# Kernel optimization log

Measured on AMD Instinct MI355X. Metric: run time of the kernel, lower is better.

Reference implementation:

```python
import jax, jax.numpy as jnp
import numpy as np


def setup_inputs() -> dict:
    key = jax.random.key(0)
    ks = jax.random.split(key, 6)
    B, T, S, E, D = 8, 128, 512, 512, 512  # batch, trg_len, src_len, enc_dim, trg_dim
    W_SCALE = 0.03  # small init to keep tanh unsaturated
    return {
        "hidden": jax.random.normal(ks[0], (B, T, D), jnp.float32),
        "encoder_outputs": jax.random.normal(ks[1], (B, S, E), jnp.float32),
        "encoder_mask": jnp.ones((B, S), jnp.float32),
        "W_attn": jax.random.normal(ks[2], (D, E + D), jnp.float32) * W_SCALE,
        "b_attn": jnp.zeros((D,), jnp.float32),
        "W_v": jax.random.normal(ks[3], (1, D), jnp.float32) * W_SCALE,
        "b_v": jnp.zeros((1,), jnp.float32),
        "W_out": jax.random.normal(ks[4], (D, E + D), jnp.float32) * W_SCALE,
    }


def masked_softmax(x, m, axis=-1):
    # faithful to repo: x*m, stable exp, e*m, normalize with eps
    x = x * m
    e_x = jnp.exp(x - jnp.max(x, axis=axis, keepdims=True))
    e_x = e_x * m
    return e_x / (jnp.sum(e_x, axis=axis, keepdims=True) + 1e-6)


def reference(hidden, encoder_outputs, encoder_mask, W_attn, b_attn, W_v, b_v, W_out):
    B, T, D = hidden.shape
    S = encoder_outputs.shape[1]
    # concat order in get_energy is (hidden_i, encoder_outputs), so split W_attn
    W_h = W_attn[:, :D]   # (D_out, trg_dim)
    W_e = W_attn[:, D:]   # (D_out, enc_dim)
    # Linear(concat) == h@W_h^T + e@W_e^T + b; vectorized over all (t, s) pairs
    hp = jnp.einsum('btd,kd->btk', hidden, W_h)            # (B,T,K)
    ep = jnp.einsum('bse,ke->bsk', encoder_outputs, W_e)   # (B,S,K)
    feat = jnp.tanh(hp[:, :, None, :] + ep[:, None, :, :] + b_attn)  # (B,T,S,K)
    energies = jnp.einsum('btsk,k->bts', feat, W_v[0]) + b_v[0]      # (B,T,S)
    # forward: energies * mask, then masked softmax
    m = encoder_mask[:, None, :]  # (B,1,S)
    energies = energies * m
    attn_weights = masked_softmax(energies, m, axis=-1)    # (B,T,S)
    weighted_context = jnp.einsum('bts,bse->bte', attn_weights, encoder_outputs)
    h_cat = jnp.concatenate([weighted_context, hidden], axis=-1)  # (B,T,E+D)
    h_tilde = jnp.tanh(jnp.einsum('btc,dc->btd', h_cat, W_out))   # (B,T,D)
    return h_tilde, weighted_context, attn_weights
```

## Files before the change

### kernel.cpp

```cpp
#include <hip/hip_runtime.h>
#include <hip/hip_bf16.h>
#include <math.h>

typedef unsigned short u16;
typedef unsigned int u32;
typedef __bf16 bf16x8 __attribute__((ext_vector_type(8)));
typedef float f32x4 __attribute__((ext_vector_type(4)));

#define OUT_WC   524288LL
#define OUT_ATTN 1048576LL
#define C2 2.8853900817779268f
#define LOG2E 1.4426950408889634f
#define LAS 40

__device__ inline u16 f2b(float f) {
    return (u16)((__float_as_uint(f) + 0x8000u) >> 16);
}
__device__ inline u32 pkcvt(float x, float y) {
    __hip_bfloat162 h = __float22bfloat162_rn(make_float2(x, y));
    return *(u32*)&h;
}
__device__ inline float tanh_fast(float x) {
    return 1.f - 2.f * __builtin_amdgcn_rcpf(__builtin_amdgcn_exp2f(C2 * x) + 1.f);
}

__global__ __launch_bounds__(256) void tobf(
    const float* __restrict__ enc, const float* __restrict__ hidden,
    const float* __restrict__ Wattn, const float* __restrict__ Wout,
    u16* __restrict__ dst)
{
    long long i = ((long long)blockIdx.x * 256 + threadIdx.x) * 8;
    const float* src; long long off;
    if (i < 2097152)      { src = enc;    off = i; }
    else if (i < 2621440) { src = hidden; off = i - 2097152; }
    else if (i < 3145728) { src = Wattn;  off = i - 2621440; }
    else                  { src = Wout;   off = i - 3145728; }
    float4 v0 = *(const float4*)(src + off);
    float4 v1 = *(const float4*)(src + off + 4);
    *(uint4*)(dst + i) = make_uint4(pkcvt(v0.x, v0.y), pkcvt(v0.z, v0.w),
                                    pkcvt(v1.x, v1.y), pkcvt(v1.z, v1.w));
}

__global__ __launch_bounds__(256) void proj(
    const u16* __restrict__ hidden_bf, const u16* __restrict__ enc_bf,
    const u16* __restrict__ Wattn_bf, const float* __restrict__ battn,
    const u16* __restrict__ Wout_bf,
    float* __restrict__ hp, u16* __restrict__ ept, float* __restrict__ hh)
{
    __shared__ u16 lA[64 * LAS];
    __shared__ u16 lB[64 * LAS];
    const int tid = threadIdx.x;
    const int wvi = tid >> 6, ln = tid & 63;
    const int wm = wvi >> 1, wn = wvi & 1;
    const int l16 = ln & 15, quad = ln >> 4;
    const int blk = blockIdx.x;
    int bx, by, zz = 0, lda, ldb, mode;
    const u16 *A, *B;
    if (blk < 512) {
        mode = 0;
        zz = blk >> 6; by = (blk >> 3) & 7; bx = blk & 7;
        A = Wattn_bf + 512; lda = 1024;
        B = enc_bf + (long long)zz * 262144; ldb = 512;
    } else if (blk < 640) {
        mode = 1;
        int i = blk - 512; by = i >> 3; bx = i & 7;
        A = hidden_bf; lda = 512;
        B = Wattn_bf; ldb = 1024;
    } else {
        mode = 2;
        int i = blk - 640; by = i >> 3; bx = i & 7;
        A = hidden_bf; lda = 512;
        B = Wout_bf + 512; ldb = 1024;
    }
    const int m0 = by * 64, n0 = bx * 64;
    const int srow = tid >> 2, skof = (tid & 3) * 8;
    const u16* Ap = A + (long long)(m0 + srow) * lda + skof;
    const u16* Bp = B + (long long)(n0 + srow) * ldb + skof;

    f32x4 acc00 = {0,0,0,0}, acc01 = {0,0,0,0}, acc10 = {0,0,0,0}, acc11 = {0,0,0,0};

    for (int k0 = 0; k0 < 512; k0 += 32) {
        uint4 av = *(const uint4*)(Ap + k0);
        uint4 bv = *(const uint4*)(Bp + k0);
        __syncthreads();
        *(uint4*)&lA[srow * LAS + skof] = av;
        *(uint4*)&lB[srow * LAS + skof] = bv;
        __syncthreads();
        bf16x8 a0 = *(const bf16x8*)&lA[(wm * 32      + l16) * LAS + quad * 8];
        bf16x8 a1 = *(const bf16x8*)&lA[(wm * 32 + 16 + l16) * LAS + quad * 8];
        bf16x8 b0 = *(const bf16x8*)&lB[(wn * 32      + l16) * LAS + quad * 8];
        bf16x8 b1 = *(const bf16x8*)&lB[(wn * 32 + 16 + l16) * LAS + quad * 8];
        acc00 = __builtin_amdgcn_mfma_f32_16x16x32_bf16(a0, b0, acc00, 0, 0, 0);
        acc01 = __builtin_amdgcn_mfma_f32_16x16x32_bf16(a0, b1, acc01, 0, 0, 0);
        acc10 = __builtin_amdgcn_mfma_f32_16x16x32_bf16(a1, b0, acc10, 0, 0, 0);
        acc11 = __builtin_amdgcn_mfma_f32_16x16x32_bf16(a1, b1, acc11, 0, 0, 0);
    }

    const f32x4* accs[4] = { &acc00, &acc01, &acc10, &acc11 };
    #pragma unroll
    for (int i = 0; i < 2; ++i) {
        #pragma unroll
        for (int j = 0; j < 2; ++j) {
            const f32x4& a = *accs[i * 2 + j];
            #pragma unroll
            for (int r = 0; r < 4; ++r) {
                int m = m0 + wm * 32 + i * 16 + quad * 4 + r;
                int n = n0 + wn * 32 + j * 16 + l16;
                float v = a[r];
                if (mode == 0)
                    ept[(long long)zz * 262144 + (long long)m * 512 + n] =
                        f2b(__builtin_amdgcn_exp2f(C2 * v));
                else if (mode == 1)
                    hp[(long long)m * 512 + n] = C2 * (v + battn[n]);
                else
                    hh[(long long)m * 512 + n] = v;
            }
        }
    }
}

__device__ inline float wred_sum(float v) {
    #pragma unroll
    for (int i = 32; i > 0; i >>= 1) v += __shfl_xor(v, i);
    return v;
}
__device__ inline float wred_max(float v) {
    #pragma unroll
    for (int i = 32; i > 0; i >>= 1) v = fmaxf(v, __shfl_xor(v, i));
    return v;
}

__device__ inline void proc8p(uint4 c0, uint4 c1, float4 hw0, float4 hw1,
                              float* a0, float* a1) {
    u32 p[4] = {c0.x, c0.y, c0.z, c0.w};
    u32 q[4] = {c1.x, c1.y, c1.z, c1.w};
    #pragma unroll
    for (int i = 0; i < 4; ++i) {
        float x0l = __uint_as_float(p[i] << 16);
        float x0h = __uint_as_float(p[i] & 0xFFFF0000u);
        float x1l = __uint_as_float(q[i] << 16);
        float x1h = __uint_as_float(q[i] & 0xFFFF0000u);
        float A, B, num;
        A = fmaf(hw0.x, x0l, 1.f);
        B = fmaf(hw1.x, x1l, 1.f);
        num = fmaf(hw0.z, B, hw1.z * A);
        a0[2*i]   = fmaf(num, __builtin_amdgcn_rcpf(A * B), a0[2*i]);
        A = fmaf(hw0.x, x0h, 1.f);
        B = fmaf(hw1.x, x1h, 1.f);
        num = fmaf(hw0.z, B, hw1.z * A);
        a0[2*i+1] = fmaf(num, __builtin_amdgcn_rcpf(A * B), a0[2*i+1]);
        A = fmaf(hw0.y, x0l, 1.f);
        B = fmaf(hw1.y, x1l, 1.f);
        num = fmaf(hw0.z, B, hw1.z * A);
        a1[2*i]   = fmaf(num, __builtin_amdgcn_rcpf(A * B), a1[2*i]);
        A = fmaf(hw0.y, x0h, 1.f);
        B = fmaf(hw1.y, x1h, 1.f);
        num = fmaf(hw0.z, B, hw1.z * A);
        a1[2*i+1] = fmaf(num, __builtin_amdgcn_rcpf(A * B), a1[2*i+1]);
    }
}
__device__ inline void wcproc2(uint4 c, float2 ap, float* acc0, float* acc1) {
    u32 cc[4] = {c.x, c.y, c.z, c.w};
    #pragma unroll
    for (int i = 0; i < 4; ++i) {
        float el = __uint_as_float(cc[i] << 16);
        float eh = __uint_as_float(cc[i] & 0xFFFF0000u);
        acc0[2*i]   = fmaf(ap.x, el, acc0[2*i]);
        acc0[2*i+1] = fmaf(ap.x, eh, acc0[2*i+1]);
        acc1[2*i]   = fmaf(ap.y, el, acc1[2*i]);
        acc1[2*i+1] = fmaf(ap.y, eh, acc1[2*i+1]);
    }
}

__global__ __launch_bounds__(1024) void energies(
    const float* __restrict__ maskp, const float* __restrict__ hp,
    const u16* __restrict__ ept, const float* __restrict__ Wv,
    const float* __restrict__ bvp, const u16* __restrict__ enc_bf,
    float* __restrict__ attn, float* __restrict__ wc)
{
    __shared__ __align__(16) float4 hpw[512];
    __shared__ float pa[2][16][512];
    __shared__ float aL[512][2];
    __shared__ float red[16];
    const int tid = threadIdx.x;
    const int b  = blockIdx.x & 7;
    const int t0 = (blockIdx.x >> 3) * 2;
    const int th = tid >> 9;
    const int k5 = tid & 511;
    const long long row0 = (long long)(b * 128 + t0) * 512;

    float hv = hp[row0 + (long long)th * 512 + k5];
    float eh = __builtin_amdgcn_exp2f(hv);
    float* hpwf = (float*)hpw;
    hpwf[k5 * 4 + th] = eh;
    float w = 0.f;
    if (th == 0) { w = Wv[k5]; hpwf[k5 * 4 + 2] = w; }
    float wsum = wred_sum(w);
    if ((tid & 63) == 0) red[tid >> 6] = wsum;
    __syncthreads();
    float sumWv = 0.f;
    #pragma unroll
    for (int i = 0; i < 16; ++i) sumWv += red[i];

    const int kg = tid >> 6, sl = tid & 63;
    const int s0 = sl * 8;
    const u16* eb = ept + (long long)b * 262144 + (kg * 32) * 512 + s0;
    const float4* hq = &hpw[kg * 32];

    float a0[8] = {0,0,0,0,0,0,0,0}, a1[8] = {0,0,0,0,0,0,0,0};
    uint4 c0 = *(const uint4*)(eb);
    uint4 c1 = *(const uint4*)(eb + 512);
    for (int kk = 0; kk < 30; kk += 2) {
        const u16* nb = eb + (kk + 2) * 512;
        uint4 n0 = *(const uint4*)(nb);
        uint4 n1 = *(const uint4*)(nb + 512);
        proc8p(c0, c1, hq[kk], hq[kk + 1], a0, a1);
        c0 = n0; c1 = n1;
    }
    proc8p(c0, c1, hq[30], hq[31], a0, a1);

    *(float4*)&pa[0][kg][s0]     = make_float4(a0[0], a0[1], a0[2], a0[3]);
    *(float4*)&pa[0][kg][s0 + 4] = make_float4(a0[4], a0[5], a0[6], a0[7]);
    *(float4*)&pa[1][kg][s0]     = make_float4(a1[0], a1[1], a1[2], a1[3]);
    *(float4*)&pa[1][kg][s0 + 4] = make_float4(a1[4], a1[5], a1[6], a1[7]);
    __syncthreads();

    float A = 0.f;
    #pragma unroll
    for (int g = 0; g < 16; ++g) A += pa[th][g][k5];
    float mv = maskp[(long long)b * 512 + k5];
    float bv0 = bvp[0];
    float r = (bv0 + sumWv - 2.f * A) * mv; r *= mv;

    float vmax = wred_max(r);
    if ((tid & 63) == 0) red[tid >> 6] = vmax;
    __syncthreads();
    float mx = red[th * 8];
    #pragma unroll
    for (int i = 1; i < 8; ++i) mx = fmaxf(mx, red[th * 8 + i]);

    float ex = __builtin_amdgcn_exp2f((r - mx) * LOG2E) * mv;
    float vsum = wred_sum(ex);
    __syncthreads();
    if ((tid & 63) == 0) red[tid >> 6] = vsum;
    __syncthreads();
    float sm = 0.f;
    #pragma unroll
    for (int i = 0; i < 8; ++i) sm += red[th * 8 + i];
    float at = ex * (1.f / (sm + 1e-6f));
    attn[row0 + (long long)th * 512 + k5] = at;
    aL[k5][th] = at;
    __syncthreads();

    const int eg = tid & 63, sg = tid >> 6;
    const u16* encb = enc_bf + (long long)b * 262144 + (long long)(sg * 32) * 512 + eg * 8;
    const float2* aq = (const float2*)&aL[sg * 32][0];
    float acc0[8] = {0,0,0,0,0,0,0,0}, acc1[8] = {0,0,0,0,0,0,0,0};
    uint4 e0 = *(const uint4*)(encb);
    uint4 e1 = *(const uint4*)(encb + 512);
    for (int j = 0; j < 30; j += 2) {
        uint4 f0 = *(const uint4*)(encb + (long long)(j + 2) * 512);
        uint4 f1 = *(const uint4*)(encb + (long long)(j + 3) * 512);
        wcproc2(e0, aq[j],     acc0, acc1);
        wcproc2(e1, aq[j + 1], acc0, acc1);
        e0 = f0; e1 = f1;
    }
    wcproc2(e0, aq[30], acc0, acc1);
    wcproc2(e1, aq[31], acc0, acc1);

    *(float4*)&pa[0][sg][eg * 8]     = make_float4(acc0[0], acc0[1], acc0[2], acc0[3]);
    *(float4*)&pa[0][sg][eg * 8 + 4] = make_float4(acc0[4], acc0[5], acc0[6], acc0[7]);
    *(float4*)&pa[1][sg][eg * 8]     = make_float4(acc1[0], acc1[1], acc1[2], acc1[3]);
    *(float4*)&pa[1][sg][eg * 8 + 4] = make_float4(acc1[4], acc1[5], acc1[6], acc1[7]);
    __syncthreads();

    float wcv = 0.f;
    #pragma unroll
    for (int g = 0; g < 16; ++g) wcv += pa[th][g][k5];
    wc[row0 + (long long)th * 512 + k5] = wcv;
}

__global__ __launch_bounds__(256) void hout_k(
    const float* __restrict__ wc, const u16* __restrict__ Wout_bf,
    float* __restrict__ out)
{
    __shared__ u16 lA[32 * LAS];
    __shared__ u16 lB[64 * LAS];
    const int tid = threadIdx.x;
    const int wvi = tid >> 6, ln = tid & 63;
    const int l16 = ln & 15, quad = ln >> 4;
    const int msub = wvi & 1, npair = wvi >> 1;
    const int m0 = blockIdx.y * 32, n0 = blockIdx.x * 64;
    const int rowA = tid >> 3, kofA = (tid & 7) * 4;
    const int rowB = tid >> 2, kofB = (tid & 3) * 8;
    f32x4 acc0 = {0,0,0,0}, acc1 = {0,0,0,0};

    for (int k0 = 0; k0 < 512; k0 += 32) {
        float4 av = *(const float4*)(wc + (long long)(m0 + rowA) * 512 + k0 + kofA);
        uint4 bv = *(const uint4*)(Wout_bf + (long long)(n0 + rowB) * 1024 + k0 + kofB);
        __syncthreads();
        *(uint2*)&lA[rowA * LAS + kofA] = make_uint2(pkcvt(av.x, av.y), pkcvt(av.z, av.w));
        int kk = kofB ^ (((rowB >> 3) & 3) << 3);
        *(uint4*)&lB[rowB * LAS + kk] = bv;
        __syncthreads();
        bf16x8 a = *(const bf16x8*)&lA[(msub * 16 + l16) * LAS + quad * 8];
        int nr0 = npair * 32 + l16, nr1 = nr0 + 16;
        bf16x8 b0 = *(const bf16x8*)&lB[nr0 * LAS + (quad * 8 ^ (((nr0 >> 3) & 3) << 3))];
        bf16x8 b1 = *(const bf16x8*)&lB[nr1 * LAS + (quad * 8 ^ (((nr1 >> 3) & 3) << 3))];
        acc0 = __builtin_amdgcn_mfma_f32_16x16x32_bf16(a, b0, acc0, 0, 0, 0);
        acc1 = __builtin_amdgcn_mfma_f32_16x16x32_bf16(a, b1, acc1, 0, 0, 0);
    }
    #pragma unroll
    for (int j = 0; j < 2; ++j) {
        const f32x4& a = j ? acc1 : acc0;
        #pragma unroll
        for (int r = 0; r < 4; ++r) {
            int m = m0 + msub * 16 + quad * 4 + r;
            int n = n0 + npair * 32 + j * 16 + l16;
            long long idx = (long long)m * 512 + n;
            out[idx] = tanh_fast(a[r] + out[idx]);
        }
    }
}

extern "C" void kernel_launch(void* const* d_in, const int* in_sizes, int n_in,
                              void* d_out, int out_size, void* d_ws, size_t ws_size,
                              hipStream_t stream)
{
    const float* hidden = (const float*)d_in[0];
    const float* enc    = (const float*)d_in[1];
    const float* mask   = (const float*)d_in[2];
    const float* Wattn  = (const float*)d_in[3];
    const float* battn  = (const float*)d_in[4];
    const float* Wv     = (const float*)d_in[5];
    const float* bvp    = (const float*)d_in[6];
    const float* Wout   = (const float*)d_in[7];
    float* out = (float*)d_out;

    float* hp  = (float*)d_ws;
    u16*   ept = (u16*)((char*)d_ws + (2 << 20));
    u16*   bfp = (u16*)((char*)d_ws + (6 << 20));
    u16* enc_bf    = bfp;
    u16* hidden_bf = bfp + 2097152;
    u16* Wattn_bf  = bfp + 2621440;
    u16* Wout_bf   = bfp + 3145728;

    tobf<<<1792, 256, 0, stream>>>(enc, hidden, Wattn, Wout, bfp);
    proj<<<768, 256, 0, stream>>>(hidden_bf, enc_bf, Wattn_bf, battn, Wout_bf,
                                  hp, ept, out );
    energies<<<512, 1024, 0, stream>>>(mask, hp, ept, Wv, bvp, enc_bf,
                                       out + OUT_ATTN, out + OUT_WC);
    hout_k<<<dim3(8, 32, 1), 256, 0, stream>>>(out + OUT_WC, Wout_bf, out);
}
```

Measured before the change: 140.1 us.

## Halve energies block size and shrink shared reduction buffer

The energies kernel now runs with 512 threads per block instead of 1024. Each thread handles 64 k-rows (or s-rows) instead of 32 and owns both target rows in the softmax stage. The shared partial-sum buffer shrinks from 2x16x512 to 8x512 floats by reducing the two rows in sequence with extra barriers, and the max and sum reductions are done for both rows together. The aim is lower LDS use and shorter cross-wave reductions so more blocks fit per CU, at the cost of longer serial loops and more syncs per block.

```diff
diff --git a/kernel.cpp b/kernel.cpp
--- a/kernel.cpp
+++ b/kernel.cpp
@@ -124,10 +124,32 @@
     for (int i = 32; i > 0; i >>= 1) v += __shfl_xor(v, i);
     return v;
 }
-__device__ inline float wred_max(float v) {
-    #pragma unroll
-    for (int i = 32; i > 0; i >>= 1) v = fmaxf(v, __shfl_xor(v, i));
-    return v;
+__device__ inline void bred2_max(float v0, float v1, float* red, int tid,
+                                 float* o0, float* o1) {
+    #pragma unroll
+    for (int i = 32; i > 0; i >>= 1) {
+        v0 = fmaxf(v0, __shfl_xor(v0, i));
+        v1 = fmaxf(v1, __shfl_xor(v1, i));
+    }
+    __syncthreads();
+    if ((tid & 63) == 0) { red[tid >> 6] = v0; red[8 + (tid >> 6)] = v1; }
+    __syncthreads();
+    float a0 = red[0], a1 = red[8];
+    #pragma unroll
+    for (int i = 1; i < 8; ++i) { a0 = fmaxf(a0, red[i]); a1 = fmaxf(a1, red[8 + i]); }
+    *o0 = a0; *o1 = a1;
+}
+__device__ inline void bred2_sum(float v0, float v1, float* red, int tid,
+                                 float* o0, float* o1) {
+    #pragma unroll
+    for (int i = 32; i > 0; i >>= 1) { v0 += __shfl_xor(v0, i); v1 += __shfl_xor(v1, i); }
+    __syncthreads();
+    if ((tid & 63) == 0) { red[tid >> 6] = v0; red[8 + (tid >> 6)] = v1; }
+    __syncthreads();
+    float a0 = 0.f, a1 = 0.f;
+    #pragma unroll
+    for (int i = 0; i < 8; ++i) { a0 += red[i]; a1 += red[8 + i]; }
+    *o0 = a0; *o1 = a1;
 }
 
 __device__ inline void proc8p(uint4 c0, uint4 c1, float4 hw0, float4 hw1,
@@ -172,112 +194,112 @@
     }
 }
 
-__global__ __launch_bounds__(1024) void energies(
+__global__ __launch_bounds__(512) void energies(
     const float* __restrict__ maskp, const float* __restrict__ hp,
     const u16* __restrict__ ept, const float* __restrict__ Wv,
     const float* __restrict__ bvp, const u16* __restrict__ enc_bf,
     float* __restrict__ attn, float* __restrict__ wc)
 {
     __shared__ __align__(16) float4 hpw[512];
-    __shared__ float pa[2][16][512];
+    __shared__ float pa[8][512];
     __shared__ float aL[512][2];
     __shared__ float red[16];
     const int tid = threadIdx.x;
     const int b  = blockIdx.x & 7;
     const int t0 = (blockIdx.x >> 3) * 2;
-    const int th = tid >> 9;
-    const int k5 = tid & 511;
     const long long row0 = (long long)(b * 128 + t0) * 512;
 
-    float hv = hp[row0 + (long long)th * 512 + k5];
-    float eh = __builtin_amdgcn_exp2f(hv);
-    float* hpwf = (float*)hpw;
-    hpwf[k5 * 4 + th] = eh;
-    float w = 0.f;
-    if (th == 0) { w = Wv[k5]; hpwf[k5 * 4 + 2] = w; }
+    float hv0 = hp[row0 + tid];
+    float hv1 = hp[row0 + 512 + tid];
+    float w = Wv[tid];
+    hpw[tid] = make_float4(__builtin_amdgcn_exp2f(hv0),
+                           __builtin_amdgcn_exp2f(hv1), w, 0.f);
     float wsum = wred_sum(w);
     if ((tid & 63) == 0) red[tid >> 6] = wsum;
     __syncthreads();
     float sumWv = 0.f;
     #pragma unroll
-    for (int i = 0; i < 16; ++i) sumWv += red[i];
+    for (int i = 0; i < 8; ++i) sumWv += red[i];
 
     const int kg = tid >> 6, sl = tid & 63;
     const int s0 = sl * 8;
-    const u16* eb = ept + (long long)b * 262144 + (kg * 32) * 512 + s0;
-    const float4* hq = &hpw[kg * 32];
+    const u16* eb = ept + (long long)b * 262144 + (kg * 64) * 512 + s0;
+    const float4* hq = &hpw[kg * 64];
 
     float a0[8] = {0,0,0,0,0,0,0,0}, a1[8] = {0,0,0,0,0,0,0,0};
     uint4 c0 = *(const uint4*)(eb);
     uint4 c1 = *(const uint4*)(eb + 512);
-    for (int kk = 0; kk < 30; kk += 2) {
+    for (int kk = 0; kk < 62; kk += 2) {
         const u16* nb = eb + (kk + 2) * 512;
         uint4 n0 = *(const uint4*)(nb);
         uint4 n1 = *(const uint4*)(nb + 512);
         proc8p(c0, c1, hq[kk], hq[kk + 1], a0, a1);
         c0 = n0; c1 = n1;
     }
-    proc8p(c0, c1, hq[30], hq[31], a0, a1);
-
-    *(float4*)&pa[0][kg][s0]     = make_float4(a0[0], a0[1], a0[2], a0[3]);
-    *(float4*)&pa[0][kg][s0 + 4] = make_float4(a0[4], a0[5], a0[6], a0[7]);
-    *(float4*)&pa[1][kg][s0]     = make_float4(a1[0], a1[1], a1[2], a1[3]);
-    *(float4*)&pa[1][kg][s0 + 4] = make_float4(a1[4], a1[5], a1[6], a1[7]);
-    __syncthreads();
-
-    float A = 0.f;
-    #pragma unroll
-    for (int g = 0; g < 16; ++g) A += pa[th][g][k5];
-    float mv = maskp[(long long)b * 512 + k5];
+    proc8p(c0, c1, hq[62], hq[63], a0, a1);
+
+    *(float4*)&pa[kg][s0]     = make_float4(a0[0], a0[1], a0[2], a0[3]);
+    *(float4*)&pa[kg][s0 + 4] = make_float4(a0[4], a0[5], a0[6], a0[7]);
+    __syncthreads();
+    float A0 = 0.f, A1 = 0.f;
+    #pragma unroll
+    for (int g = 0; g < 8; ++g) A0 += pa[g][tid];
+    __syncthreads();
+    *(float4*)&pa[kg][s0]     = make_float4(a1[0], a1[1], a1[2], a1[3]);
+    *(float4*)&pa[kg][s0 + 4] = make_float4(a1[4], a1[5], a1[6], a1[7]);
+    __syncthreads();
+    #pragma unroll
+    for (int g = 0; g < 8; ++g) A1 += pa[g][tid];
+
+    const int s = tid;
+    float mv = maskp[(long long)b * 512 + s];
     float bv0 = bvp[0];
-    float r = (bv0 + sumWv - 2.f * A) * mv; r *= mv;
-
-    float vmax = wred_max(r);
-    if ((tid & 63) == 0) red[tid >> 6] = vmax;
-    __syncthreads();
-    float mx = red[th * 8];
-    #pragma unroll
-    for (int i = 1; i < 8; ++i) mx = fmaxf(mx, red[th * 8 + i]);
-
-    float ex = __builtin_amdgcn_exp2f((r - mx) * LOG2E) * mv;
-    float vsum = wred_sum(ex);
-    __syncthreads();
-    if ((tid & 63) == 0) red[tid >> 6] = vsum;
-    __syncthreads();
-    float sm = 0.f;
-    #pragma unroll
-    for (int i = 0; i < 8; ++i) sm += red[th * 8 + i];
-    float at = ex * (1.f / (sm + 1e-6f));
-    attn[row0 + (long long)th * 512 + k5] = at;
-    aL[k5][th] = at;
+    float r0 = (bv0 + sumWv - 2.f * A0) * mv; r0 *= mv;
+    float r1 = (bv0 + sumWv - 2.f * A1) * mv; r1 *= mv;
+
+    float mx0, mx1;
+    bred2_max(r0, r1, red, tid, &mx0, &mx1);
+    float ex0 = __builtin_amdgcn_exp2f((r0 - mx0) * LOG2E) * mv;
+    float ex1 = __builtin_amdgcn_exp2f((r1 - mx1) * LOG2E) * mv;
+    float sm0, sm1;
+    bred2_sum(ex0, ex1, red, tid, &sm0, &sm1);
+    float at0 = ex0 * (1.f / (sm0 + 1e-6f));
+    float at1 = ex1 * (1.f / (sm1 + 1e-6f));
+    attn[row0 + s]       = at0;
+    attn[row0 + 512 + s] = at1;
+    aL[s][0] = at0; aL[s][1] = at1;
     __syncthreads();
 
     const int eg = tid & 63, sg = tid >> 6;
-    const u16* encb = enc_bf + (long long)b * 262144 + (long long)(sg * 32) * 512 + eg * 8;
-    const float2* aq = (const float2*)&aL[sg * 32][0];
+    const u16* encb = enc_bf + (long long)b * 262144 + (long long)(sg * 64) * 512 + eg * 8;
+    const float2* aq = (const float2*)&aL[sg * 64][0];
     float acc0[8] = {0,0,0,0,0,0,0,0}, acc1[8] = {0,0,0,0,0,0,0,0};
     uint4 e0 = *(const uint4*)(encb);
     uint4 e1 = *(const uint4*)(encb + 512);
-    for (int j = 0; j < 30; j += 2) {
+    for (int j = 0; j < 62; j += 2) {
         uint4 f0 = *(const uint4*)(encb + (long long)(j + 2) * 512);
         uint4 f1 = *(const uint4*)(encb + (long long)(j + 3) * 512);
         wcproc2(e0, aq[j],     acc0, acc1);
         wcproc2(e1, aq[j + 1], acc0, acc1);
         e0 = f0; e1 = f1;
     }
-    wcproc2(e0, aq[30], acc0, acc1);
-    wcproc2(e1, aq[31], acc0, acc1);
-
-    *(float4*)&pa[0][sg][eg * 8]     = make_float4(acc0[0], acc0[1], acc0[2], acc0[3]);
-    *(float4*)&pa[0][sg][eg * 8 + 4] = make_float4(acc0[4], acc0[5], acc0[6], acc0[7]);
-    *(float4*)&pa[1][sg][eg * 8]     = make_float4(acc1[0], acc1[1], acc1[2], acc1[3]);
-    *(float4*)&pa[1][sg][eg * 8 + 4] = make_float4(acc1[4], acc1[5], acc1[6], acc1[7]);
-    __syncthreads();
-
-    float wcv = 0.f;
-    #pragma unroll
-    for (int g = 0; g < 16; ++g) wcv += pa[th][g][k5];
-    wc[row0 + (long long)th * 512 + k5] = wcv;
+    wcproc2(e0, aq[62], acc0, acc1);
+    wcproc2(e1, aq[63], acc0, acc1);
+
+    *(float4*)&pa[sg][eg * 8]     = make_float4(acc0[0], acc0[1], acc0[2], acc0[3]);
+    *(float4*)&pa[sg][eg * 8 + 4] = make_float4(acc0[4], acc0[5], acc0[6], acc0[7]);
+    __syncthreads();
+    float wcv0 = 0.f, wcv1 = 0.f;
+    #pragma unroll
+    for (int g = 0; g < 8; ++g) wcv0 += pa[g][tid];
+    __syncthreads();
+    *(float4*)&pa[sg][eg * 8]     = make_float4(acc1[0], acc1[1], acc1[2], acc1[3]);
+    *(float4*)&pa[sg][eg * 8 + 4] = make_float4(acc1[4], acc1[5], acc1[6], acc1[7]);
+    __syncthreads();
+    #pragma unroll
+    for (int g = 0; g < 8; ++g) wcv1 += pa[g][tid];
+    wc[row0 + tid]       = wcv0;
+    wc[row0 + 512 + tid] = wcv1;
 }
 
 __global__ __launch_bounds__(256) void hout_k(
@@ -348,7 +370,7 @@
     tobf<<<1792, 256, 0, stream>>>(enc, hidden, Wattn, Wout, bfp);
     proj<<<768, 256, 0, stream>>>(hidden_bf, enc_bf, Wattn_bf, battn, Wout_bf,
                                   hp, ept, out );
-    energies<<<512, 1024, 0, stream>>>(mask, hp, ept, Wv, bvp, enc_bf,
-                                       out + OUT_ATTN, out + OUT_WC);
+    energies<<<512, 512, 0, stream>>>(mask, hp, ept, Wv, bvp, enc_bf,
+                                      out + OUT_ATTN, out + OUT_WC);
     hout_k<<<dim3(8, 32, 1), 256, 0, stream>>>(out + OUT_WC, Wout_bf, out);
 }
```

Measured after the change: 137.7 us. About the same (-1.7%).
